# Kernel optimization log

Hardware: AMD Instinct MI355X
Metric: run time of the kernel (lower is better)

## Reference

```python
import jax, jax.numpy as jnp
import numpy as np

N_NODES = 100000
N_EDGES = 1600000
N_FEAT = 128
HIDDEN = 128
N_CLASSES = 8
N_GRAPHS = 256


def setup_inputs() -> dict:
    key = jax.random.key(0)
    ks = jax.random.split(key, 10)
    x = jax.random.normal(ks[0], (N_NODES, N_FEAT), dtype=jnp.float32)
    edge_index = jax.random.randint(ks[1], (2, N_EDGES), 0, N_NODES, dtype=jnp.int64)
    batch = jnp.sort(jax.random.randint(ks[2], (N_NODES,), 0, N_GRAPHS, dtype=jnp.int64))
    s = 1.0 / np.sqrt(HIDDEN)
    W1 = jax.random.normal(ks[3], (N_FEAT, HIDDEN), dtype=jnp.float32) * s
    b1 = jnp.zeros((HIDDEN,), dtype=jnp.float32)
    W2 = jax.random.normal(ks[4], (HIDDEN, HIDDEN), dtype=jnp.float32) * s
    b2 = jnp.zeros((HIDDEN,), dtype=jnp.float32)
    W3 = jax.random.normal(ks[5], (HIDDEN, HIDDEN), dtype=jnp.float32) * s
    b3 = jnp.zeros((HIDDEN,), dtype=jnp.float32)
    Wc1 = jax.random.normal(ks[6], (HIDDEN, HIDDEN // 2), dtype=jnp.float32) * s
    bc1 = jnp.zeros((HIDDEN // 2,), dtype=jnp.float32)
    Wc2 = jax.random.normal(ks[7], (HIDDEN // 2, N_CLASSES), dtype=jnp.float32) * (1.0 / np.sqrt(HIDDEN // 2))
    bc2 = jnp.zeros((N_CLASSES,), dtype=jnp.float32)
    return dict(x=x, edge_index=edge_index, batch=batch, W1=W1, b1=b1,
                W2=W2, b2=b2, W3=W3, b3=b3, Wc1=Wc1, bc1=bc1, Wc2=Wc2, bc2=bc2)


def _gcn_conv(x, W, b, src, dst, dinv_src_dst, deg_inv):
    # PyG GCNConv: h = X W; out = sum_{j->i} norm_ij * h_j + deg_i^{-1} * h_i + b
    h = x @ W  # [N, H]
    msg = h[src] * dinv_src_dst[:, None]            # gather + scale  [E, H]
    agg = jax.ops.segment_sum(msg, dst, num_segments=N_NODES)
    agg = agg + h * deg_inv[:, None]                # self-loop term
    return agg + b


def reference(x, edge_index, batch, W1, b1, W2, b2, W3, b3, Wc1, bc1, Wc2, bc2):
    src, dst = edge_index[0], edge_index[1]
    # symmetric normalization with self-loops: deg_i = 1 + in-degree
    ones = jnp.ones((N_EDGES,), dtype=x.dtype)
    deg = jax.ops.segment_sum(ones, dst, num_segments=N_NODES) + 1.0
    dinv = jax.lax.rsqrt(deg)                        # deg^{-1/2}
    dinv_src_dst = dinv[src] * dinv[dst]             # norm per edge
    deg_inv = 1.0 / deg                              # self-loop norm

    h = jax.nn.relu(_gcn_conv(x, W1, b1, src, dst, dinv_src_dst, deg_inv))
    h = jax.nn.relu(_gcn_conv(h, W2, b2, src, dst, dinv_src_dst, deg_inv))
    h = jax.nn.relu(_gcn_conv(h, W3, b3, src, dst, dinv_src_dst, deg_inv))

    # global_mean_pool over batch ids
    sums = jax.ops.segment_sum(h, batch, num_segments=N_GRAPHS)
    counts = jax.ops.segment_sum(jnp.ones((N_NODES,), dtype=h.dtype), batch,
                                 num_segments=N_GRAPHS)
    pooled = sums / jnp.maximum(counts, 1.0)[:, None]  # [G, H]

    # classifier MLP (eval mode: dropout = identity)
    z = jax.nn.relu(pooled @ Wc1 + bc1)
    return z @ Wc2 + bc2
```

## Files before the change

### kernel.cpp

```cpp
#include <hip/hip_runtime.h>
#include <hip/hip_bf16.h>

#define N_NODES 100000
#define N_EDGES 1600000
#define NFEAT   128
#define HID     128
#define NG      256
#define NCLS    8
#define ELL_CAP 64

typedef __attribute__((ext_vector_type(8))) short bf16x8;
typedef __attribute__((ext_vector_type(4))) float f32x4;

__device__ __forceinline__ unsigned short f2bf(float f) {
    unsigned u = __float_as_uint(f);
    unsigned r = (u + 0x7fffu + ((u >> 16) & 1u)) >> 16;
    return (unsigned short)r;
}


__global__ void zero_int_kernel(int* __restrict__ p, int n) {
    int i = blockIdx.x * 256 + threadIdx.x;
    if (i < n) p[i] = 0;
}

__global__ void fill_ell_kernel(const int* __restrict__ src, const int* __restrict__ dst,
                                int* __restrict__ cnt, int* __restrict__ col_ell) {
    int i = blockIdx.x * 256 + threadIdx.x;
    if (i < N_EDGES) {
        int s = src[i], d = dst[i];
        int c = atomicAdd(&cnt[d], 1);
        if (c < ELL_CAP) col_ell[(size_t)d * ELL_CAP + c] = s;
    }
}

__global__ void node_scalars_kernel(const int* __restrict__ cnt, float* __restrict__ dinv) {
    int i = blockIdx.x * 256 + threadIdx.x;
    if (i < N_NODES) dinv[i] = rsqrtf((float)cnt[i] + 1.0f);
}

__global__ void cast_w_kernel(const float* __restrict__ W1, const float* __restrict__ W2,
                              const float* __restrict__ W3,
                              unsigned short* __restrict__ T1, unsigned short* __restrict__ T2,
                              unsigned short* __restrict__ T3) {
    int b = blockIdx.x;
    const float*    W = (b < 64) ? W1 : ((b < 128) ? W2 : W3);
    unsigned short* T = (b < 64) ? T1 : ((b < 128) ? T2 : T3);
    int i = (b & 63) * 256 + threadIdx.x;
    int k = i >> 7, n = i & 127;
    T[n * 128 + k] = f2bf(W[i]);
}

__global__ __launch_bounds__(256) void gemm_mfma_kernel(
        const float* __restrict__ in, unsigned short* __restrict__ G,
        const unsigned short* __restrict__ Wt, const float* __restrict__ dinv) {
    const int tid  = threadIdx.x;
    const int wave = tid >> 6;
    const int lane = tid & 63;
    const int r16  = lane & 15;
    const int g    = lane >> 4;
    const int arow = blockIdx.x * 64 + wave * 16 + r16;
    const int arowc = (arow < N_NODES) ? arow : (N_NODES - 1);

    bf16x8 a[4];
#pragma unroll
    for (int kk = 0; kk < 4; ++kk) {
        const float* p = &in[(size_t)arowc * 128 + kk * 32 + g * 8];
        float4 lo = *(const float4*)p;
        float4 hi = *(const float4*)(p + 4);
        union { bf16x8 v; unsigned short u[8]; } t;
        t.u[0] = f2bf(lo.x); t.u[1] = f2bf(lo.y); t.u[2] = f2bf(lo.z); t.u[3] = f2bf(lo.w);
        t.u[4] = f2bf(hi.x); t.u[5] = f2bf(hi.y); t.u[6] = f2bf(hi.z); t.u[7] = f2bf(hi.w);
        a[kk] = t.v;
    }

    const bf16x8* Wv = (const bf16x8*)Wt;
    const int orow0 = blockIdx.x * 64 + wave * 16 + g * 4;

    float dv[4];
#pragma unroll
    for (int i = 0; i < 4; ++i) {
        int gr = orow0 + i;
        dv[i] = (gr < N_NODES) ? dinv[gr] : 0.f;
    }

#pragma unroll
    for (int ct = 0; ct < 8; ++ct) {
        const int nb = (ct * 16 + r16) * 16 + g;
        f32x4 acc = {0.f, 0.f, 0.f, 0.f};
#pragma unroll
        for (int kk = 0; kk < 4; ++kk)
            acc = __builtin_amdgcn_mfma_f32_16x16x32_bf16(a[kk], Wv[nb + kk * 4], acc, 0, 0, 0);
        const int col = ct * 16 + r16;
#pragma unroll
        for (int i = 0; i < 4; ++i) {
            int gr = orow0 + i;
            if (gr < N_NODES) G[(size_t)gr * 128 + col] = f2bf(acc[i] * dv[i]);
        }
    }
}

__global__ __launch_bounds__(256) void spmm_bias_relu_kernel(
        const unsigned int* __restrict__ G,
        float* __restrict__ out,
        const int* __restrict__ cnt, const int* __restrict__ col_ell,
        const float* __restrict__ dinv, const float* __restrict__ bias) {
    int wave = threadIdx.x >> 6;
    int node = blockIdx.x * 4 + wave;
    int lane = threadIdx.x & 63;
    if (node >= N_NODES) return;

    unsigned sv = G[(size_t)node * 64 + lane];
    float2 acc;
    acc.x = __uint_as_float(sv << 16);
    acc.y = __uint_as_float(sv & 0xffff0000u);

    int n = cnt[node];
    if (n > ELL_CAP) n = ELL_CAP;
    const int* cl = &col_ell[(size_t)node * ELL_CAP];
    int c = 0;
    for (; c + 1 < n; c += 2) {
        int c0 = cl[c], c1 = cl[c + 1];
        unsigned v0 = G[(size_t)c0 * 64 + lane];
        unsigned v1 = G[(size_t)c1 * 64 + lane];
        acc.x += __uint_as_float(v0 << 16);
        acc.y += __uint_as_float(v0 & 0xffff0000u);
        acc.x += __uint_as_float(v1 << 16);
        acc.y += __uint_as_float(v1 & 0xffff0000u);
    }
    if (c < n) {
        unsigned v0 = G[(size_t)cl[c] * 64 + lane];
        acc.x += __uint_as_float(v0 << 16);
        acc.y += __uint_as_float(v0 & 0xffff0000u);
    }

    float di = dinv[node];
    float2 b2 = ((const float2*)bias)[lane];
    float2 o;
    o.x = fmaxf(di * acc.x + b2.x, 0.f);
    o.y = fmaxf(di * acc.y + b2.y, 0.f);
    ((float2*)out)[(size_t)node * 64 + lane] = o;
}

__global__ __launch_bounds__(1024) void pool_kernel(const float* __restrict__ H,
                                                    const int* __restrict__ batch,
                                                    float* __restrict__ pooled) {
    __shared__ float red[8][128];
    int g = blockIdx.x;
    int t = threadIdx.x;
    int f = t & 127;
    int s = t >> 7;

    int lo = 0, hi = N_NODES;
    while (lo < hi) { int mid = (lo + hi) >> 1; if (batch[mid] < g) lo = mid + 1; else hi = mid; }
    int start = lo;
    lo = start; hi = N_NODES;
    while (lo < hi) { int mid = (lo + hi) >> 1; if (batch[mid] < g + 1) lo = mid + 1; else hi = mid; }
    int end = lo;

    float acc = 0.f;
    for (int n = start + s; n < end; n += 8) acc += H[(size_t)n * 128 + f];
    red[s][f] = acc;
    __syncthreads();
    if (s == 0) {
        float v = ((red[0][f] + red[1][f]) + (red[2][f] + red[3][f]))
                + ((red[4][f] + red[5][f]) + (red[6][f] + red[7][f]));
        float cnt = (float)(end - start);
        pooled[g * 128 + f] = v / fmaxf(cnt, 1.0f);
    }
}

__global__ void classify_kernel(const float* __restrict__ pooled,
                                const float* __restrict__ Wc1, const float* __restrict__ bc1,
                                const float* __restrict__ Wc2, const float* __restrict__ bc2,
                                float* __restrict__ out) {
    __shared__ float p[128];
    __shared__ float z[64];
    int g = blockIdx.x;
    int t = threadIdx.x;
    p[t]      = pooled[g * 128 + t];
    p[t + 64] = pooled[g * 128 + t + 64];
    __syncthreads();
    float a = bc1[t];
#pragma unroll 4
    for (int k = 0; k < 128; ++k) a += p[k] * Wc1[k * 64 + t];
    z[t] = fmaxf(a, 0.f);
    __syncthreads();
    if (t < 8) {
        float o = bc2[t];
#pragma unroll 8
        for (int j = 0; j < 64; ++j) o += z[j] * Wc2[j * 8 + t];
        out[g * 8 + t] = o;
    }
}


extern "C" void kernel_launch(void* const* d_in, const int* in_sizes, int n_in,
                              void* d_out, int out_size, void* d_ws, size_t ws_size,
                              hipStream_t stream) {
    const float* x    = (const float*)d_in[0];
    const int*   ei   = (const int*)d_in[1];
    const int*   bat  = (const int*)d_in[2];
    const float* W1   = (const float*)d_in[3];
    const float* b1   = (const float*)d_in[4];
    const float* W2   = (const float*)d_in[5];
    const float* b2   = (const float*)d_in[6];
    const float* W3   = (const float*)d_in[7];
    const float* b3   = (const float*)d_in[8];
    const float* Wc1  = (const float*)d_in[9];
    const float* bc1  = (const float*)d_in[10];
    const float* Wc2  = (const float*)d_in[11];
    const float* bc2  = (const float*)d_in[12];
    float* out = (float*)d_out;

    const int* src = ei;
    const int* dst = ei + N_EDGES;

    char* base = (char*)d_ws;
    size_t off = 0;
    auto alloc = [&](size_t bytes) -> void* {
        void* p = base + off;
        off = (off + bytes + 255) & ~(size_t)255;
        return p;
    };
    int*            cnt     = (int*)           alloc((size_t)N_NODES * 4);
    float*          dinv    = (float*)         alloc((size_t)N_NODES * 4);
    int*            col_ell = (int*)           alloc((size_t)N_NODES * ELL_CAP * 4);
    float*          bufA    = (float*)         alloc((size_t)N_NODES * 128 * 4);
    unsigned short* bufG    = (unsigned short*)alloc((size_t)N_NODES * 128 * 2);
    float*          pooled  = (float*)         alloc((size_t)NG * 128 * 4);
    unsigned short* Wt1     = (unsigned short*)alloc((size_t)HID * HID * 2);
    unsigned short* Wt2     = (unsigned short*)alloc((size_t)HID * HID * 2);
    unsigned short* Wt3     = (unsigned short*)alloc((size_t)HID * HID * 2);
    (void)ws_size; (void)n_in; (void)in_sizes; (void)out_size;

    const int nTilesN  = (N_NODES + 255) / 256;
    const int nBlocksE = (N_EDGES + 255) / 256;

    hipLaunchKernelGGL(cast_w_kernel, dim3(192), dim3(256), 0, stream, W1, W2, W3, Wt1, Wt2, Wt3);
    hipLaunchKernelGGL(zero_int_kernel, dim3(nTilesN), dim3(256), 0, stream, cnt, N_NODES);
    hipLaunchKernelGGL(fill_ell_kernel, dim3(nBlocksE), dim3(256), 0, stream, src, dst, cnt, col_ell);
    hipLaunchKernelGGL(node_scalars_kernel, dim3(nTilesN), dim3(256), 0, stream, cnt, dinv);

    const int gemmGrid = (N_NODES + 63) / 64;
    const int spmmGrid = N_NODES / 4;

    hipLaunchKernelGGL(gemm_mfma_kernel, dim3(gemmGrid), dim3(256), 0, stream, x, bufG, Wt1, dinv);
    hipLaunchKernelGGL(spmm_bias_relu_kernel, dim3(spmmGrid), dim3(256), 0, stream,
                       (const unsigned int*)bufG, bufA, cnt, col_ell, dinv, b1);
    hipLaunchKernelGGL(gemm_mfma_kernel, dim3(gemmGrid), dim3(256), 0, stream, bufA, bufG, Wt2, dinv);
    hipLaunchKernelGGL(spmm_bias_relu_kernel, dim3(spmmGrid), dim3(256), 0, stream,
                       (const unsigned int*)bufG, bufA, cnt, col_ell, dinv, b2);
    hipLaunchKernelGGL(gemm_mfma_kernel, dim3(gemmGrid), dim3(256), 0, stream, bufA, bufG, Wt3, dinv);
    hipLaunchKernelGGL(spmm_bias_relu_kernel, dim3(spmmGrid), dim3(256), 0, stream,
                       (const unsigned int*)bufG, bufA, cnt, col_ell, dinv, b3);

    hipLaunchKernelGGL(pool_kernel, dim3(NG), dim3(1024), 0, stream, bufA, bat, pooled);
    hipLaunchKernelGGL(classify_kernel, dim3(NG), dim3(64), 0, stream, pooled, Wc1, bc1, Wc2, bc2, out);
}
```

Baseline: 680.8 us.

## Fuse ELL build with first GEMM and move source scaling into SpMM

Drops the dinv scaling from the GEMM epilogue so the first-layer GEMM no longer waits on the degree computation. The ELL fill and the layer-1 GEMM then run in one horizontally fused launch. The SpMM now gathers dinv[src] per neighbor and applies it before accumulating, and its loop is unrolled by four. This saves one launch and overlaps the atomic-heavy fill with MFMA work, at the cost of an extra per-edge scalar gather in all three SpMM passes.

```diff
diff --git a/kernel.cpp b/kernel.cpp
--- a/kernel.cpp
+++ b/kernel.cpp
@@ -8,6 +8,8 @@
 #define NG      256
 #define NCLS    8
 #define ELL_CAP 64
+#define FILL_BLOCKS 6250
+#define GEMM_BLOCKS 1563
 
 typedef __attribute__((ext_vector_type(8))) short bf16x8;
 typedef __attribute__((ext_vector_type(4))) float f32x4;
@@ -17,21 +19,13 @@
     unsigned r = (u + 0x7fffu + ((u >> 16) & 1u)) >> 16;
     return (unsigned short)r;
 }
+__device__ __forceinline__ float bf_lo(unsigned v) { return __uint_as_float(v << 16); }
+__device__ __forceinline__ float bf_hi(unsigned v) { return __uint_as_float(v & 0xffff0000u); }
 
 
 __global__ void zero_int_kernel(int* __restrict__ p, int n) {
     int i = blockIdx.x * 256 + threadIdx.x;
     if (i < n) p[i] = 0;
-}
-
-__global__ void fill_ell_kernel(const int* __restrict__ src, const int* __restrict__ dst,
-                                int* __restrict__ cnt, int* __restrict__ col_ell) {
-    int i = blockIdx.x * 256 + threadIdx.x;
-    if (i < N_EDGES) {
-        int s = src[i], d = dst[i];
-        int c = atomicAdd(&cnt[d], 1);
-        if (c < ELL_CAP) col_ell[(size_t)d * ELL_CAP + c] = s;
-    }
 }
 
 __global__ void node_scalars_kernel(const int* __restrict__ cnt, float* __restrict__ dinv) {
@@ -51,15 +45,15 @@
     T[n * 128 + k] = f2bf(W[i]);
 }
 
-__global__ __launch_bounds__(256) void gemm_mfma_kernel(
-        const float* __restrict__ in, unsigned short* __restrict__ G,
-        const unsigned short* __restrict__ Wt, const float* __restrict__ dinv) {
+__device__ __forceinline__ void gemm_body(int bid, const float* __restrict__ in,
+                                          unsigned short* __restrict__ H,
+                                          const unsigned short* __restrict__ Wt) {
     const int tid  = threadIdx.x;
     const int wave = tid >> 6;
     const int lane = tid & 63;
     const int r16  = lane & 15;
     const int g    = lane >> 4;
-    const int arow = blockIdx.x * 64 + wave * 16 + r16;
+    const int arow = bid * 64 + wave * 16 + r16;
     const int arowc = (arow < N_NODES) ? arow : (N_NODES - 1);
 
     bf16x8 a[4];
@@ -75,14 +69,7 @@
     }
 
     const bf16x8* Wv = (const bf16x8*)Wt;
-    const int orow0 = blockIdx.x * 64 + wave * 16 + g * 4;
-
-    float dv[4];
-#pragma unroll
-    for (int i = 0; i < 4; ++i) {
-        int gr = orow0 + i;
-        dv[i] = (gr < N_NODES) ? dinv[gr] : 0.f;
-    }
+    const int orow0 = bid * 64 + wave * 16 + g * 4;
 
 #pragma unroll
     for (int ct = 0; ct < 8; ++ct) {
@@ -95,13 +82,37 @@
 #pragma unroll
         for (int i = 0; i < 4; ++i) {
             int gr = orow0 + i;
-            if (gr < N_NODES) G[(size_t)gr * 128 + col] = f2bf(acc[i] * dv[i]);
+            if (gr < N_NODES) H[(size_t)gr * 128 + col] = f2bf(acc[i]);
         }
     }
 }
 
+__global__ __launch_bounds__(256) void build_gemm1_kernel(
+        const int* __restrict__ src, const int* __restrict__ dst,
+        int* __restrict__ cnt, int* __restrict__ col_ell,
+        const float* __restrict__ x, unsigned short* __restrict__ H,
+        const unsigned short* __restrict__ Wt1) {
+    int b = blockIdx.x;
+    if (b < FILL_BLOCKS) {
+        int i = b * 256 + threadIdx.x;
+        if (i < N_EDGES) {
+            int s = src[i], d = dst[i];
+            int c = atomicAdd(&cnt[d], 1);
+            if (c < ELL_CAP) col_ell[(size_t)d * ELL_CAP + c] = s;
+        }
+    } else {
+        gemm_body(b - FILL_BLOCKS, x, H, Wt1);
+    }
+}
+
+__global__ __launch_bounds__(256) void gemm_mfma_kernel(
+        const float* __restrict__ in, unsigned short* __restrict__ H,
+        const unsigned short* __restrict__ Wt) {
+    gemm_body(blockIdx.x, in, H, Wt);
+}
+
 __global__ __launch_bounds__(256) void spmm_bias_relu_kernel(
-        const unsigned int* __restrict__ G,
+        const unsigned int* __restrict__ H,
         float* __restrict__ out,
         const int* __restrict__ cnt, const int* __restrict__ col_ell,
         const float* __restrict__ dinv, const float* __restrict__ bias) {
@@ -110,31 +121,36 @@
     int lane = threadIdx.x & 63;
     if (node >= N_NODES) return;
 
-    unsigned sv = G[(size_t)node * 64 + lane];
+    float di = dinv[node];
+    unsigned sv = H[(size_t)node * 64 + lane];
     float2 acc;
-    acc.x = __uint_as_float(sv << 16);
-    acc.y = __uint_as_float(sv & 0xffff0000u);
+    acc.x = di * bf_lo(sv);
+    acc.y = di * bf_hi(sv);
 
     int n = cnt[node];
     if (n > ELL_CAP) n = ELL_CAP;
     const int* cl = &col_ell[(size_t)node * ELL_CAP];
     int c = 0;
-    for (; c + 1 < n; c += 2) {
-        int c0 = cl[c], c1 = cl[c + 1];
-        unsigned v0 = G[(size_t)c0 * 64 + lane];
-        unsigned v1 = G[(size_t)c1 * 64 + lane];
-        acc.x += __uint_as_float(v0 << 16);
-        acc.y += __uint_as_float(v0 & 0xffff0000u);
-        acc.x += __uint_as_float(v1 << 16);
-        acc.y += __uint_as_float(v1 & 0xffff0000u);
-    }
-    if (c < n) {
-        unsigned v0 = G[(size_t)cl[c] * 64 + lane];
-        acc.x += __uint_as_float(v0 << 16);
-        acc.y += __uint_as_float(v0 & 0xffff0000u);
-    }
-
-    float di = dinv[node];
+    for (; c + 3 < n; c += 4) {
+        int c0 = cl[c], c1 = cl[c + 1], c2 = cl[c + 2], c3 = cl[c + 3];
+        float w0 = dinv[c0], w1 = dinv[c1], w2 = dinv[c2], w3 = dinv[c3];
+        unsigned v0 = H[(size_t)c0 * 64 + lane];
+        unsigned v1 = H[(size_t)c1 * 64 + lane];
+        unsigned v2 = H[(size_t)c2 * 64 + lane];
+        unsigned v3 = H[(size_t)c3 * 64 + lane];
+        acc.x += w0 * bf_lo(v0) + w1 * bf_lo(v1);
+        acc.y += w0 * bf_hi(v0) + w1 * bf_hi(v1);
+        acc.x += w2 * bf_lo(v2) + w3 * bf_lo(v3);
+        acc.y += w2 * bf_hi(v2) + w3 * bf_hi(v3);
+    }
+    for (; c < n; ++c) {
+        int c0 = cl[c];
+        float w0 = dinv[c0];
+        unsigned v0 = H[(size_t)c0 * 64 + lane];
+        acc.x += w0 * bf_lo(v0);
+        acc.y += w0 * bf_hi(v0);
+    }
+
     float2 b2 = ((const float2*)bias)[lane];
     float2 o;
     o.x = fmaxf(di * acc.x + b2.x, 0.f);
@@ -227,33 +243,32 @@
     float*          dinv    = (float*)         alloc((size_t)N_NODES * 4);
     int*            col_ell = (int*)           alloc((size_t)N_NODES * ELL_CAP * 4);
     float*          bufA    = (float*)         alloc((size_t)N_NODES * 128 * 4);
-    unsigned short* bufG    = (unsigned short*)alloc((size_t)N_NODES * 128 * 2);
+    unsigned short* bufH    = (unsigned short*)alloc((size_t)N_NODES * 128 * 2);
     float*          pooled  = (float*)         alloc((size_t)NG * 128 * 4);
     unsigned short* Wt1     = (unsigned short*)alloc((size_t)HID * HID * 2);
     unsigned short* Wt2     = (unsigned short*)alloc((size_t)HID * HID * 2);
     unsigned short* Wt3     = (unsigned short*)alloc((size_t)HID * HID * 2);
     (void)ws_size; (void)n_in; (void)in_sizes; (void)out_size;
 
-    const int nTilesN  = (N_NODES + 255) / 256;
-    const int nBlocksE = (N_EDGES + 255) / 256;
+    const int nTilesN = (N_NODES + 255) / 256;
 
     hipLaunchKernelGGL(cast_w_kernel, dim3(192), dim3(256), 0, stream, W1, W2, W3, Wt1, Wt2, Wt3);
     hipLaunchKernelGGL(zero_int_kernel, dim3(nTilesN), dim3(256), 0, stream, cnt, N_NODES);
-    hipLaunchKernelGGL(fill_ell_kernel, dim3(nBlocksE), dim3(256), 0, stream, src, dst, cnt, col_ell);
+
+    hipLaunchKernelGGL(build_gemm1_kernel, dim3(FILL_BLOCKS + GEMM_BLOCKS), dim3(256), 0, stream,
+                       src, dst, cnt, col_ell, x, bufH, Wt1);
     hipLaunchKernelGGL(node_scalars_kernel, dim3(nTilesN), dim3(256), 0, stream, cnt, dinv);
 
-    const int gemmGrid = (N_NODES + 63) / 64;
     const int spmmGrid = N_NODES / 4;
 
-    hipLaunchKernelGGL(gemm_mfma_kernel, dim3(gemmGrid), dim3(256), 0, stream, x, bufG, Wt1, dinv);
     hipLaunchKernelGGL(spmm_bias_relu_kernel, dim3(spmmGrid), dim3(256), 0, stream,
-                       (const unsigned int*)bufG, bufA, cnt, col_ell, dinv, b1);
-    hipLaunchKernelGGL(gemm_mfma_kernel, dim3(gemmGrid), dim3(256), 0, stream, bufA, bufG, Wt2, dinv);
+                       (const unsigned int*)bufH, bufA, cnt, col_ell, dinv, b1);
+    hipLaunchKernelGGL(gemm_mfma_kernel, dim3(GEMM_BLOCKS), dim3(256), 0, stream, bufA, bufH, Wt2);
     hipLaunchKernelGGL(spmm_bias_relu_kernel, dim3(spmmGrid), dim3(256), 0, stream,
-                       (const unsigned int*)bufG, bufA, cnt, col_ell, dinv, b2);
-    hipLaunchKernelGGL(gemm_mfma_kernel, dim3(gemmGrid), dim3(256), 0, stream, bufA, bufG, Wt3, dinv);
+                       (const unsigned int*)bufH, bufA, cnt, col_ell, dinv, b2);
+    hipLaunchKernelGGL(gemm_mfma_kernel, dim3(GEMM_BLOCKS), dim3(256), 0, stream, bufA, bufH, Wt3);
     hipLaunchKernelGGL(spmm_bias_relu_kernel, dim3(spmmGrid), dim3(256), 0, stream,
-                       (const unsigned int*)bufG, bufA, cnt, col_ell, dinv, b3);
+                       (const unsigned int*)bufH, bufA, cnt, col_ell, dinv, b3);
 
     hipLaunchKernelGGL(pool_kernel, dim3(NG), dim3(1024), 0, stream, bufA, bat, pooled);
     hipLaunchKernelGGL(classify_kernel, dim3(NG), dim3(64), 0, stream, pooled, Wc1, bc1, Wc2, bc2, out);
```

New measurement: 621.4 us. 8.7% less time.
